# Kernel tuning notes

Hardware: AMD Instinct MI355X
Metric: run time of the kernel (lower is better)

## Reference

```python
import jax, jax.numpy as jnp
import numpy as np

N_HEADS = 16
D_HEAD = 64
IGNORE = -100000.0


def setup_inputs() -> dict:
    key = jax.random.key(0)
    ks = jax.random.split(key, 5)
    B, S, D = 2, 2048, 1024
    return {
        "residual": jax.random.normal(ks[0], (B, S, D), dtype=jnp.float32),
        "q": jax.random.normal(ks[1], (B, S, D), dtype=jnp.float32),
        "k": jax.random.normal(ks[2], (B, S, D), dtype=jnp.float32),
        "v": jax.random.normal(ks[3], (B, S, D), dtype=jnp.float32),
        "W_O": jax.random.normal(ks[4], (N_HEADS, D_HEAD, D), dtype=jnp.float32) * 0.02,
        "b_O": jnp.zeros((D,), dtype=jnp.float32),
    }


def reference(residual, q, k, v, W_O, b_O):
    B, S, _ = q.shape
    attn_scale = np.sqrt(D_HEAD).astype(np.float32)  # use_attn_scale=True
    # split heads: [..., pos, (h d)] -> [..., pos, h, d]
    qh = q.reshape(B, S, N_HEADS, D_HEAD)
    kh = k.reshape(B, S, N_HEADS, D_HEAD)
    vh = v.reshape(B, S, N_HEADS, D_HEAD)
    # scores: [..., head, query_pos, key_pos]
    scores = jnp.einsum("bqhd,bkhd->bhqk", qh, kh) / attn_scale
    causal = jnp.tril(jnp.ones((S, S), dtype=bool))
    scores = jnp.where(causal, scores, jnp.float32(IGNORE))
    pattern = jax.nn.softmax(scores, axis=-1)
    # weighted sum of values: [..., query_pos, head, d_head]
    z = jnp.einsum("bkhd,bhqk->bqhd", vh, pattern)
    out = jnp.einsum("bqhd,hdm->bqm", z, W_O) + b_O
    return (residual, out)
```

## Files before the change

### kernel.cpp

```cpp
#include <hip/hip_runtime.h>

#define B_ 2
#define S_ 2048
#define D_ 1024
#define H_ 16
#define DH_ 64
#define NP_ 2048

typedef short v8s __attribute__((ext_vector_type(8)));
typedef float v4f __attribute__((ext_vector_type(4)));
typedef float v16f __attribute__((ext_vector_type(16)));
typedef unsigned int v2u __attribute__((ext_vector_type(2)));
typedef unsigned int v4u __attribute__((ext_vector_type(4)));
typedef unsigned int uint32;

__device__ inline short f2bf(float f) {
  unsigned u = __float_as_uint(f);
  u = (u + 0x7FFFu + ((u >> 16) & 1u)) >> 16;
  return (short)u;
}

__device__ inline unsigned pk_bf16(float lo, float hi) {
  unsigned r;
  asm("v_cvt_pk_bf16_f32 %0, %1, %2" : "=v"(r) : "v"(lo), "v"(hi));
  return r;
}

__device__ inline void gll16(const void* g, void* l) {
  __builtin_amdgcn_global_load_lds(
      (const __attribute__((address_space(1))) void*)g,
      (__attribute__((address_space(3))) void*)l, 16, 0, 0);
}

__global__ __launch_bounds__(256) void cvt_bf16_kernel(const float* __restrict__ in,
                                                       short* __restrict__ out) {
  int i = blockIdx.x * blockDim.x + threadIdx.x;
  float4 a = ((const float4*)in)[2 * i];
  float4 b = ((const float4*)in)[2 * i + 1];
  v8s t;
  t[0] = f2bf(a.x); t[1] = f2bf(a.y); t[2] = f2bf(a.z); t[3] = f2bf(a.w);
  t[4] = f2bf(b.x); t[5] = f2bf(b.y); t[6] = f2bf(b.z); t[7] = f2bf(b.w);
  ((v8s*)out)[i] = t;
}

__global__ __launch_bounds__(256) void cvt_vt_kernel(const float* __restrict__ v,
                                                     short* __restrict__ vt) {
  int bid = blockIdx.x;
  int st = bid & 31;
  int bh = bid >> 5;
  int b = bh >> 4, h = bh & 15;
  int tid = threadIdx.x;
  __shared__ short t[64][64 + 8];
  int r = tid >> 2, c16 = (tid & 3) * 16;
  const float* vp = v + ((size_t)(b * S_ + st * 64 + r)) * D_ + h * DH_ + c16;
  for (int i = 0; i < 16; i += 4) {
    float4 a = *(const float4*)(vp + i);
    t[r][c16 + i + 0] = f2bf(a.x);
    t[r][c16 + i + 1] = f2bf(a.y);
    t[r][c16 + i + 2] = f2bf(a.z);
    t[r][c16 + i + 3] = f2bf(a.w);
  }
  __syncthreads();
  short* op = vt + ((size_t)((b * H_ + h) * DH_ + r)) * S_ + st * 64 + c16;
  v8s o0, o1;
  for (int j = 0; j < 8; ++j) { o0[j] = t[c16 + j][r]; o1[j] = t[c16 + 8 + j][r]; }
  *(v8s*)op = o0;
  *(v8s*)(op + 8) = o1;
}

__global__ __launch_bounds__(256) void cvt_wt_kernel(const float* __restrict__ w,
                                                     short* __restrict__ wt) {
  int bid = blockIdx.x;
  int tk = bid & 15, tm = bid >> 4;
  int tid = threadIdx.x;
  __shared__ short t[64][64 + 8];
  int r = tid >> 2, c16 = (tid & 3) * 16;
  const float* wp = w + (size_t)(tk * 64 + r) * D_ + tm * 64 + c16;
  for (int i = 0; i < 16; i += 4) {
    float4 a = *(const float4*)(wp + i);
    t[r][c16 + i + 0] = f2bf(a.x);
    t[r][c16 + i + 1] = f2bf(a.y);
    t[r][c16 + i + 2] = f2bf(a.z);
    t[r][c16 + i + 3] = f2bf(a.w);
  }
  __syncthreads();
  short* op = wt + (size_t)(tm * 64 + r) * D_ + tk * 64 + c16;
  v8s o0, o1;
  for (int j = 0; j < 8; ++j) { o0[j] = t[c16 + j][r]; o1[j] = t[c16 + 8 + j][r]; }
  *(v8s*)op = o0;
  *(v8s*)(op + 8) = o1;
}

template <int SPLITS>
__global__ __launch_bounds__(128, 4) void attn_kernel(
    const float* __restrict__ q, const short* __restrict__ kbf,
    const short* __restrict__ vtb, uint32* __restrict__ Opart,
    float* __restrict__ Lsum) {
  constexpr int SHIFT = (SPLITS == 2 ? 6 : 5);
  int bid = blockIdx.x;
  int bh = bid & 31;
  int sp = (SPLITS == 2) ? ((bid >> 5) & 1) : 0;
  int qt = 31 - (int)(bid >> SHIFT);
  int b = bh >> 4, h = bh & 15;

  int nt = qt + 1;
  int hs = (nt + 1) >> 1;
  int t0 = (SPLITS == 2 && sp == 1) ? hs : 0;
  int t1 = (SPLITS == 2 && sp == 0) ? hs - 1 : qt;

  int tid = threadIdx.x;
  int wave = tid >> 6, lane = tid & 63;
  int l31 = lane & 31, h32 = lane >> 5;

  __shared__ short Klds[64][64];
  __shared__ short Vlds[64][64];

  const int qrow0 = qt * 64 + wave * 32;
  const int lr8 = lane >> 3;
  const int scol = ((lane & 7) ^ lr8) << 3;

  const short* pk_ = kbf + (size_t)b * S_ * D_ + h * DH_ +
                     (size_t)(t0 * 64 + wave * 8 + lr8) * D_ + scol;
  const short* pv_ = vtb + (size_t)(b * H_ + h) * DH_ * S_ +
                     (size_t)(wave * 8 + lr8) * S_ + t0 * 64 + scol;

  v8s qf[4];
  {
    const float* qp = q + (size_t)(b * S_ + qrow0 + l31) * D_ + h * DH_ + h32 * 8;
    const float sc = 0.125f * 1.44269504f;
#pragma unroll
    for (int d4 = 0; d4 < 4; ++d4) {
      float4 x = *(const float4*)(qp + d4 * 16);
      float4 y = *(const float4*)(qp + d4 * 16 + 4);
      v8s tq;
      tq[0] = f2bf(x.x * sc); tq[1] = f2bf(x.y * sc);
      tq[2] = f2bf(x.z * sc); tq[3] = f2bf(x.w * sc);
      tq[4] = f2bf(y.x * sc); tq[5] = f2bf(y.y * sc);
      tq[6] = f2bf(y.z * sc); tq[7] = f2bf(y.w * sc);
      qf[d4] = tq;
    }
  }

  v16f O0, O1;
#pragma unroll
  for (int r = 0; r < 16; ++r) { O0[r] = 0.f; O1[r] = 0.f; }
  float L = 0.f;
  const int swz = (l31 & 7) << 3;

  for (int s = t0; s <= t1; ++s) {
#pragma unroll
    for (int i = 0; i < 4; ++i)
      gll16(pk_ + (size_t)(i * 16) * D_, &Klds[i * 16 + wave * 8][0]);
#pragma unroll
    for (int i = 0; i < 4; ++i)
      gll16(pv_ + (size_t)(i * 16) * S_, &Vlds[i * 16 + wave * 8][0]);
    pk_ += (size_t)64 * D_;
    pv_ += 64;
    asm volatile("s_waitcnt vmcnt(0)" ::: "memory");
    __builtin_amdgcn_sched_barrier(0);
    __builtin_amdgcn_s_barrier();
    __builtin_amdgcn_sched_barrier(0);

    int kb = s * 64;
    bool skip1 = (kb >= qrow0);
    bool msk = (kb + 63 > qrow0);

    __builtin_amdgcn_s_setprio(1);
    v16f S0, S1;
#pragma unroll
    for (int r = 0; r < 16; ++r) { S0[r] = 0.f; S1[r] = 0.f; }
#pragma unroll
    for (int d4 = 0; d4 < 4; ++d4) {
      v8s kf = *(const v8s*)&Klds[l31][(((d4 << 1) | h32) << 3) ^ swz];
      S0 = __builtin_amdgcn_mfma_f32_32x32x16_bf16(kf, qf[d4], S0, 0, 0, 0);
    }
    if (!skip1) {
#pragma unroll
      for (int d4 = 0; d4 < 4; ++d4) {
        v8s kf = *(const v8s*)&Klds[32 + l31][(((d4 << 1) | h32) << 3) ^ swz];
        S1 = __builtin_amdgcn_mfma_f32_32x32x16_bf16(kf, qf[d4], S1, 0, 0, 0);
      }
    }
    __builtin_amdgcn_s_setprio(0);

    int qg = qrow0 + l31;
    if (msk) {
#pragma unroll
      for (int r = 0; r < 16; ++r) {
        int kl = kb + (r & 3) + 8 * (r >> 2) + 4 * h32;
        if (kl > qg) S0[r] = -1e30f;
      }
      if (!skip1) {
#pragma unroll
        for (int r = 0; r < 16; ++r) {
          int kl = kb + 32 + (r & 3) + 8 * (r >> 2) + 4 * h32;
          if (kl > qg) S1[r] = -1e30f;
        }
      }
    }

    float rs = 0.f;
    unsigned pw0[8], pw1[8];
#pragma unroll
    for (int r = 0; r < 16; ++r) {
      S0[r] = __builtin_amdgcn_exp2f(S0[r]);
      rs += S0[r];
    }
#pragma unroll
    for (int w = 0; w < 8; ++w) pw0[w] = pk_bf16(S0[2 * w], S0[2 * w + 1]);
    if (!skip1) {
#pragma unroll
      for (int r = 0; r < 16; ++r) {
        S1[r] = __builtin_amdgcn_exp2f(S1[r]);
        rs += S1[r];
      }
#pragma unroll
      for (int w = 0; w < 8; ++w) pw1[w] = pk_bf16(S1[2 * w], S1[2 * w + 1]);
    }
    rs += __shfl_xor(rs, 32);
    L += rs;

    __builtin_amdgcn_s_setprio(1);
#pragma unroll
    for (int ks = 0; ks < 2; ++ks) {
      v2u a = __builtin_amdgcn_permlane32_swap(pw0[ks * 4 + 0], pw0[ks * 4 + 2], false, false);
      v2u c = __builtin_amdgcn_permlane32_swap(pw0[ks * 4 + 1], pw0[ks * 4 + 3], false, false);
      v4u fw; fw.x = a.x; fw.y = c.x; fw.z = a.y; fw.w = c.y;
      v8s pb = __builtin_bit_cast(v8s, fw);
      v8s vf0 = *(const v8s*)&Vlds[l31][(((ks << 1) | h32) << 3) ^ swz];
      O0 = __builtin_amdgcn_mfma_f32_32x32x16_bf16(vf0, pb, O0, 0, 0, 0);
      v8s vf1 = *(const v8s*)&Vlds[32 + l31][(((ks << 1) | h32) << 3) ^ swz];
      O1 = __builtin_amdgcn_mfma_f32_32x32x16_bf16(vf1, pb, O1, 0, 0, 0);
    }
    if (!skip1) {
#pragma unroll
      for (int ks = 0; ks < 2; ++ks) {
        v2u a = __builtin_amdgcn_permlane32_swap(pw1[ks * 4 + 0], pw1[ks * 4 + 2], false, false);
        v2u c = __builtin_amdgcn_permlane32_swap(pw1[ks * 4 + 1], pw1[ks * 4 + 3], false, false);
        v4u fw; fw.x = a.x; fw.y = c.x; fw.z = a.y; fw.w = c.y;
        v8s pb = __builtin_bit_cast(v8s, fw);
        v8s vf0 = *(const v8s*)&Vlds[l31][((((ks + 2) << 1) | h32) << 3) ^ swz];
        O0 = __builtin_amdgcn_mfma_f32_32x32x16_bf16(vf0, pb, O0, 0, 0, 0);
        v8s vf1 = *(const v8s*)&Vlds[32 + l31][((((ks + 2) << 1) | h32) << 3) ^ swz];
        O1 = __builtin_amdgcn_mfma_f32_32x32x16_bf16(vf1, pb, O1, 0, 0, 0);
      }
    }
    __builtin_amdgcn_s_setprio(0);

    __builtin_amdgcn_sched_barrier(0);
    __builtin_amdgcn_s_barrier();
    __builtin_amdgcn_sched_barrier(0);
  }

  int p = bh * 64 + qt * 2 + wave;
  uint32* Op = Opart + ((size_t)(sp * NP_ + p)) * 1024;
#pragma unroll
  for (int w = 0; w < 8; ++w) {
    int dpair = 4 * (w >> 1) + (w & 1) + 2 * h32;
    Op[dpair * 32 + l31] = pk_bf16(O0[2 * w], O0[2 * w + 1]);
    Op[(16 + dpair) * 32 + l31] = pk_bf16(O1[2 * w], O1[2 * w + 1]);
  }
  if (h32 == 0) Lsum[(size_t)(sp * NP_ + p) * 32 + l31] = L;
}

template <int SPLITS>
__global__ __launch_bounds__(128) void merge_kernel(
    const uint32* __restrict__ Opart, const float* __restrict__ Lsum,
    short* __restrict__ z) {
  int p = blockIdx.x;
  int tid = threadIdx.x;
  int qq = tid & 31, g = tid >> 5;

  float Lt = Lsum[(size_t)p * 32 + qq];
  if constexpr (SPLITS == 2) Lt += Lsum[(size_t)(NP_ + p) * 32 + qq];
  float f = 1.f / Lt;

  __shared__ uint32 T[32][33];
  const uint32* O0 = Opart + (size_t)p * 1024;
  const uint32* O1 = Opart + (size_t)(NP_ + p) * 1024;
#pragma unroll
  for (int j = 0; j < 8; ++j) {
    int dp = g * 8 + j;
    uint32 u0 = O0[dp * 32 + qq];
    float lo = __uint_as_float(u0 << 16);
    float hi = __uint_as_float(u0 & 0xFFFF0000u);
    if constexpr (SPLITS == 2) {
      uint32 u1 = O1[dp * 32 + qq];
      lo += __uint_as_float(u1 << 16);
      hi += __uint_as_float(u1 & 0xFFFF0000u);
    }
    T[qq][dp] = pk_bf16(lo * f, hi * f);
  }
  __syncthreads();
  int q2 = tid >> 2, c = (tid & 3) * 8;
  int srow = (p & 63) * 32 + q2;
  int b = p >> 10, h = (p >> 6) & 15;
  uint32* zp = (uint32*)z + ((size_t)(b * S_ + srow)) * (D_ / 2) + h * 32 + c;
#pragma unroll
  for (int j = 0; j < 8; ++j) zp[j] = T[q2][c + j];
}

__global__ __launch_bounds__(256) void proj_kernel(
    const short* __restrict__ z, const short* __restrict__ wt,
    const float* __restrict__ bias, float* __restrict__ out) {
  int bm = blockIdx.x, bn = blockIdx.y;
  int tid = threadIdx.x;
  int wave = tid >> 6, lane = tid & 63, lh = lane >> 4, ll = lane & 15;
  int wr = wave >> 1, wc = wave & 1;

  __shared__ short Al[2][64][64];
  __shared__ short Bl[2][128][64];

  const int r8 = lane >> 3;
  const int scol = ((lane & 7) ^ r8) << 3;

  v4f acc[2][4];
#pragma unroll
  for (int m = 0; m < 2; ++m)
#pragma unroll
    for (int n = 0; n < 4; ++n) acc[m][n] = (v4f){0.f, 0.f, 0.f, 0.f};

  auto stage = [&](int kb, int bbuf) {
#pragma unroll
    for (int i = 0; i < 2; ++i) {
      int c = wave * 2 + i;
      gll16(z + (size_t)(bm * 64 + c * 8 + r8) * D_ + kb + scol, &Al[bbuf][c * 8][0]);
    }
#pragma unroll
    for (int i = 0; i < 4; ++i) {
      int c = wave * 4 + i;
      gll16(wt + (size_t)(bn * 128 + c * 8 + r8) * D_ + kb + scol, &Bl[bbuf][c * 8][0]);
    }
  };

  stage(0, 0);
  __syncthreads();

  for (int kt = 0; kt < D_ / 64; ++kt) {
    int bbuf = kt & 1;
    if (kt + 1 < D_ / 64) stage((kt + 1) * 64, bbuf ^ 1);
    v8s af[2][2], bf[4][2];
#pragma unroll
    for (int m = 0; m < 2; ++m) {
      int row = wr * 32 + m * 16 + ll;
#pragma unroll
      for (int c = 0; c < 2; ++c)
        af[m][c] = *(const v8s*)&Al[bbuf][row][(((c << 2) | lh) ^ (ll & 7)) << 3];
    }
#pragma unroll
    for (int n = 0; n < 4; ++n) {
      int row = wc * 64 + n * 16 + ll;
#pragma unroll
      for (int c = 0; c < 2; ++c)
        bf[n][c] = *(const v8s*)&Bl[bbuf][row][(((c << 2) | lh) ^ (ll & 7)) << 3];
    }
#pragma unroll
    for (int m = 0; m < 2; ++m)
#pragma unroll
      for (int n = 0; n < 4; ++n)
#pragma unroll
        for (int c = 0; c < 2; ++c)
          acc[m][n] = __builtin_amdgcn_mfma_f32_16x16x32_bf16(af[m][c], bf[n][c], acc[m][n], 0, 0, 0);
    __syncthreads();
  }

#pragma unroll
  for (int m = 0; m < 2; ++m) {
    int gr = bm * 64 + wr * 32 + m * 16 + lh * 4;
#pragma unroll
    for (int n = 0; n < 4; ++n) {
      int gc = bn * 128 + wc * 64 + n * 16 + ll;
      float bo = bias[gc];
#pragma unroll
      for (int r = 0; r < 4; ++r)
        out[(size_t)(gr + r) * D_ + gc] = acc[m][n][r] + bo;
    }
  }
}

extern "C" void kernel_launch(void* const* d_in, const int* in_sizes, int n_in,
                              void* d_out, int out_size, void* d_ws, size_t ws_size,
                              hipStream_t stream) {
  const float* residual = (const float*)d_in[0];
  const float* q = (const float*)d_in[1];
  const float* k = (const float*)d_in[2];
  const float* v = (const float*)d_in[3];
  const float* W = (const float*)d_in[4];
  const float* bO = (const float*)d_in[5];
  float* out = (float*)d_out;

  const size_t half = (size_t)B_ * S_ * D_;
  char* ws = (char*)d_ws;
  short* z = (short*)ws;
  short* kbf = z + half;
  short* vtb = kbf + half;
  short* wtb = vtb + half;
  char* pbase = (char*)(wtb + (size_t)D_ * D_);
  const size_t opart_b = (size_t)NP_ * 1024 * 4;
  const size_t l_b = (size_t)NP_ * 32 * 4;
  const size_t base_b = (size_t)pbase - (size_t)ws;

  hipMemcpyAsync(out, residual, half * sizeof(float), hipMemcpyDeviceToDevice, stream);

  cvt_bf16_kernel<<<half / 2048, 256, 0, stream>>>(k, kbf);
  cvt_vt_kernel<<<B_ * H_ * (S_ / 64), 256, 0, stream>>>(v, vtb);
  cvt_wt_kernel<<<(D_ / 64) * (D_ / 64), 256, 0, stream>>>(W, wtb);

  if (ws_size >= base_b + 2 * (opart_b + l_b)) {
    uint32* Opart = (uint32*)pbase;
    float* Lsum = (float*)(pbase + 2 * opart_b);
    attn_kernel<2><<<2048, 128, 0, stream>>>(q, kbf, vtb, Opart, Lsum);
    merge_kernel<2><<<NP_, 128, 0, stream>>>(Opart, Lsum, z);
  } else {
    uint32* Opart = (uint32*)pbase;
    float* Lsum = (float*)(pbase + opart_b);
    attn_kernel<1><<<1024, 128, 0, stream>>>(q, kbf, vtb, Opart, Lsum);
    merge_kernel<1><<<NP_, 128, 0, stream>>>(Opart, Lsum, z);
  }

  proj_kernel<<<dim3((B_ * S_) / 64, D_ / 128), 256, 0, stream>>>(z, wtb, bO, out + half);
}
```

Measured before the change: 77.09 us.

## Fuse split merge into projection GEMM and residual copy into attention

Removes the separate merge kernel. The projection GEMM now reads the bf16 partial outputs and softmax sums directly, normalises them, and writes the A tile into shared memory with software prefetch. The residual passthrough copy moves from a hipMemcpyAsync into the tail of the attention kernel. This saves one launch, the z intermediate round trip and the memcpy. In exchange, each projection block re-reads Opart for every N tile (8x redundant merge work), and the attention kernel does extra memory traffic at its end.

Result: faster. 75.49 us (-2.1%).

```diff
diff --git a/kernel.cpp b/kernel.cpp
--- a/kernel.cpp
+++ b/kernel.cpp
@@ -95,7 +95,8 @@
 __global__ __launch_bounds__(128, 4) void attn_kernel(
     const float* __restrict__ q, const short* __restrict__ kbf,
     const short* __restrict__ vtb, uint32* __restrict__ Opart,
-    float* __restrict__ Lsum) {
+    float* __restrict__ Lsum, const float* __restrict__ residual,
+    float* __restrict__ res_out) {
   constexpr int SHIFT = (SPLITS == 2 ? 6 : 5);
   int bid = blockIdx.x;
   int bh = bid & 31;
@@ -261,48 +262,22 @@
     Op[(16 + dpair) * 32 + l31] = pk_bf16(O1[2 * w], O1[2 * w + 1]);
   }
   if (h32 == 0) Lsum[(size_t)(sp * NP_ + p) * 32 + l31] = L;
+
+  {
+    constexpr int F4 = (SPLITS == 2) ? 4 : 8;
+    const float4* rs_ = (const float4*)residual;
+    float4* rd_ = (float4*)res_out;
+    size_t base = (size_t)bid * (128 * F4) + tid;
+#pragma unroll
+    for (int j = 0; j < F4; ++j) rd_[base + j * 128] = rs_[base + j * 128];
+  }
 }
 
 template <int SPLITS>
-__global__ __launch_bounds__(128) void merge_kernel(
+__global__ __launch_bounds__(256) void proj_kernel(
     const uint32* __restrict__ Opart, const float* __restrict__ Lsum,
-    short* __restrict__ z) {
-  int p = blockIdx.x;
-  int tid = threadIdx.x;
-  int qq = tid & 31, g = tid >> 5;
-
-  float Lt = Lsum[(size_t)p * 32 + qq];
-  if constexpr (SPLITS == 2) Lt += Lsum[(size_t)(NP_ + p) * 32 + qq];
-  float f = 1.f / Lt;
-
-  __shared__ uint32 T[32][33];
-  const uint32* O0 = Opart + (size_t)p * 1024;
-  const uint32* O1 = Opart + (size_t)(NP_ + p) * 1024;
-#pragma unroll
-  for (int j = 0; j < 8; ++j) {
-    int dp = g * 8 + j;
-    uint32 u0 = O0[dp * 32 + qq];
-    float lo = __uint_as_float(u0 << 16);
-    float hi = __uint_as_float(u0 & 0xFFFF0000u);
-    if constexpr (SPLITS == 2) {
-      uint32 u1 = O1[dp * 32 + qq];
-      lo += __uint_as_float(u1 << 16);
-      hi += __uint_as_float(u1 & 0xFFFF0000u);
-    }
-    T[qq][dp] = pk_bf16(lo * f, hi * f);
-  }
-  __syncthreads();
-  int q2 = tid >> 2, c = (tid & 3) * 8;
-  int srow = (p & 63) * 32 + q2;
-  int b = p >> 10, h = (p >> 6) & 15;
-  uint32* zp = (uint32*)z + ((size_t)(b * S_ + srow)) * (D_ / 2) + h * 32 + c;
-#pragma unroll
-  for (int j = 0; j < 8; ++j) zp[j] = T[q2][c + j];
-}
-
-__global__ __launch_bounds__(256) void proj_kernel(
-    const short* __restrict__ z, const short* __restrict__ wt,
-    const float* __restrict__ bias, float* __restrict__ out) {
+    const short* __restrict__ wt, const float* __restrict__ bias,
+    float* __restrict__ out) {
   int bm = blockIdx.x, bn = blockIdx.y;
   int tid = threadIdx.x;
   int wave = tid >> 6, lane = tid & 63, lh = lane >> 4, ll = lane & 15;
@@ -314,45 +289,88 @@
   const int r8 = lane >> 3;
   const int scol = ((lane & 7) ^ r8) << 3;
 
+  const int sq = tid & 31;
+  const int sph = tid >> 7;
+  const int sdg = (tid >> 5) & 3;
+  const int srow = sph * 32 + sq;
+  const int sx7 = srow & 7;
+
+  const int b = bm >> 5, qt = bm & 31;
+  const size_t prow = (size_t)(b * 16) * 64 + qt * 2 + sph;
+
   v4f acc[2][4];
 #pragma unroll
   for (int m = 0; m < 2; ++m)
 #pragma unroll
     for (int n = 0; n < 4; ++n) acc[m][n] = (v4f){0.f, 0.f, 0.f, 0.f};
 
-  auto stage = [&](int kb, int bbuf) {
-#pragma unroll
-    for (int i = 0; i < 2; ++i) {
-      int c = wave * 2 + i;
-      gll16(z + (size_t)(bm * 64 + c * 8 + r8) * D_ + kb + scol, &Al[bbuf][c * 8][0]);
-    }
+  uint32 a0[8], a1[8];
+  float f;
+
+  auto loadA = [&](int kt) {
+    size_t p = prow + (size_t)kt * 64;
+    const uint32* src = Opart + p * 1024 + (sdg * 8) * 32 + sq;
+#pragma unroll
+    for (int j = 0; j < 8; ++j) a0[j] = src[j * 32];
+    if constexpr (SPLITS == 2) {
+      const uint32* src1 = src + (size_t)NP_ * 1024;
+#pragma unroll
+      for (int j = 0; j < 8; ++j) a1[j] = src1[j * 32];
+    }
+    float Lt = Lsum[p * 32 + sq];
+    if constexpr (SPLITS == 2) Lt += Lsum[((size_t)NP_ + p) * 32 + sq];
+    f = 1.f / Lt;
+  };
+
+  auto writeA = [&](int buf) {
+#pragma unroll
+    for (int j = 0; j < 8; ++j) {
+      int dp = sdg * 8 + j;
+      float lo = __uint_as_float(a0[j] << 16);
+      float hi = __uint_as_float(a0[j] & 0xFFFF0000u);
+      if constexpr (SPLITS == 2) {
+        lo += __uint_as_float(a1[j] << 16);
+        hi += __uint_as_float(a1[j] & 0xFFFF0000u);
+      }
+      uint32 w = pk_bf16(lo * f, hi * f);
+      int g = dp >> 2;
+      *(uint32*)&Al[buf][srow][(((g ^ sx7) << 3) + ((dp & 3) << 1))] = w;
+    }
+  };
+
+  auto stageB = [&](int kb, int buf) {
 #pragma unroll
     for (int i = 0; i < 4; ++i) {
       int c = wave * 4 + i;
-      gll16(wt + (size_t)(bn * 128 + c * 8 + r8) * D_ + kb + scol, &Bl[bbuf][c * 8][0]);
+      gll16(wt + (size_t)(bn * 128 + c * 8 + r8) * D_ + kb + scol, &Bl[buf][c * 8][0]);
     }
   };
 
-  stage(0, 0);
+  loadA(0);
+  stageB(0, 0);
+  writeA(0);
   __syncthreads();
 
-  for (int kt = 0; kt < D_ / 64; ++kt) {
-    int bbuf = kt & 1;
-    if (kt + 1 < D_ / 64) stage((kt + 1) * 64, bbuf ^ 1);
+  for (int kt = 0; kt < 16; ++kt) {
+    int buf = kt & 1;
+    if (kt + 1 < 16) {
+      loadA(kt + 1);
+      stageB((kt + 1) * 64, buf ^ 1);
+    }
     v8s af[2][2], bf[4][2];
 #pragma unroll
     for (int m = 0; m < 2; ++m) {
       int row = wr * 32 + m * 16 + ll;
 #pragma unroll
       for (int c = 0; c < 2; ++c)
-        af[m][c] = *(const v8s*)&Al[bbuf][row][(((c << 2) | lh) ^ (ll & 7)) << 3];
+        af[m][c] = *(const v8s*)&Al[buf][row][(((c << 2) | lh) ^ (ll & 7)) << 3];
     }
 #pragma unroll
     for (int n = 0; n < 4; ++n) {
       int row = wc * 64 + n * 16 + ll;
 #pragma unroll
       for (int c = 0; c < 2; ++c)
-        bf[n][c] = *(const v8s*)&Bl[bbuf][row][(((c << 2) | lh) ^ (ll & 7)) << 3];
+        bf[n][c] = *(const v8s*)&Bl[buf][row][(((c << 2) | lh) ^ (ll & 7)) << 3];
     }
 #pragma unroll
     for (int m = 0; m < 2; ++m)
@@ -361,6 +379,7 @@
 #pragma unroll
         for (int c = 0; c < 2; ++c)
           acc[m][n] = __builtin_amdgcn_mfma_f32_16x16x32_bf16(af[m][c], bf[n][c], acc[m][n], 0, 0, 0);
+    if (kt + 1 < 16) writeA(buf ^ 1);
     __syncthreads();
   }
 
@@ -391,8 +410,7 @@
 
   const size_t half = (size_t)B_ * S_ * D_;
   char* ws = (char*)d_ws;
-  short* z = (short*)ws;
-  short* kbf = z + half;
+  short* kbf = (short*)ws;
   short* vtb = kbf + half;
   short* wtb = vtb + half;
   char* pbase = (char*)(wtb + (size_t)D_ * D_);
@@ -400,8 +418,6 @@
   const size_t l_b = (size_t)NP_ * 32 * 4;
   const size_t base_b = (size_t)pbase - (size_t)ws;
 
-  hipMemcpyAsync(out, residual, half * sizeof(float), hipMemcpyDeviceToDevice, stream);
-
   cvt_bf16_kernel<<<half / 2048, 256, 0, stream>>>(k, kbf);
   cvt_vt_kernel<<<B_ * H_ * (S_ / 64), 256, 0, stream>>>(v, vtb);
   cvt_wt_kernel<<<(D_ / 64) * (D_ / 64), 256, 0, stream>>>(W, wtb);
@@ -409,14 +425,14 @@
   if (ws_size >= base_b + 2 * (opart_b + l_b)) {
     uint32* Opart = (uint32*)pbase;
     float* Lsum = (float*)(pbase + 2 * opart_b);
-    attn_kernel<2><<<2048, 128, 0, stream>>>(q, kbf, vtb, Opart, Lsum);
-    merge_kernel<2><<<NP_, 128, 0, stream>>>(Opart, Lsum, z);
+    attn_kernel<2><<<2048, 128, 0, stream>>>(q, kbf, vtb, Opart, Lsum, residual, out);
+    proj_kernel<2><<<dim3((B_ * S_) / 64, D_ / 128), 256, 0, stream>>>(
+        Opart, Lsum, wtb, bO, out + half);
   } else {
     uint32* Opart = (uint32*)pbase;
     float* Lsum = (float*)(pbase + opart_b);
-    attn_kernel<1><<<1024, 128, 0, stream>>>(q, kbf, vtb, Opart, Lsum);
-    merge_kernel<1><<<NP_, 128, 0, stream>>>(Opart, Lsum, z);
-  }
-
-  proj_kernel<<<dim3((B_ * S_) / 64, D_ / 128), 256, 0, stream>>>(z, wtb, bO, out + half);
-}
+    attn_kernel<1><<<1024, 128, 0, stream>>>(q, kbf, vtb, Opart, Lsum, residual, out);
+    proj_kernel<1><<<dim3((B_ * S_) / 64, D_ / 128), 256, 0, stream>>>(
+        Opart, Lsum, wtb, bO, out + half);
+  }
+}
```
